# Optimization experiments

Measured on AMD Instinct MI355X. Metric: run time of the kernel, lower is better.

## Reference

```python
import jax, jax.numpy as jnp
import numpy as np

B, N, D, F = 4, 50000, 8, 128

def setup_inputs() -> dict:
    key = jax.random.key(0)
    ks = jax.random.split(key, 6)
    x = jax.random.normal(ks[0], (B, N, F), dtype=jnp.float32)
    adj = jax.random.randint(ks[1], (N, D), 0, N, dtype=jnp.int32)
    # torch.nn.Linear weights: [out_features, in_features], in = 2*F
    W1 = jax.random.normal(ks[2], (F, 2 * F), dtype=jnp.float32) * 0.05
    b1 = jax.random.normal(ks[3], (F,), dtype=jnp.float32) * 0.05
    W2 = jax.random.normal(ks[4], (F, 2 * F), dtype=jnp.float32) * 0.05
    b2 = jax.random.normal(ks[5], (F,), dtype=jnp.float32) * 0.05
    return {"x": x, "adj": adj, "W1": W1, "b1": b1, "W2": W2, "b2": b2}

def _gnn_layer(x, adj, W, b):
    # x: [B, N, F]; adj: [N, D]
    nb = x[:, adj, :]                 # [B, N, D, F] irregular gather
    agg = jnp.max(nb, axis=2)         # max-aggregate over neighbors -> [B, N, F]
    cc = jnp.concatenate([agg, x], axis=-1)  # [B, N, 2F]
    return jax.nn.relu(jnp.einsum('bnf,of->bno', cc, W) + b)

def reference(x, adj, W1, b1, W2, b2):
    x = _gnn_layer(x, adj, W1, b1)
    x = _gnn_layer(x, adj, W2, b2)
    return x
```

## Files before the change

### kernel.cpp

```cpp
#include <hip/hip_runtime.h>


#define N_NODES 50000
#define N_BATCH 4
#define DEG 8
#define FDIM 128
#define K2 256
#define TILE_M 64

typedef _Float16 f16x8 __attribute__((ext_vector_type(8)));
typedef _Float16 f16x4 __attribute__((ext_vector_type(4)));
typedef float f32x4 __attribute__((ext_vector_type(4)));

__global__ void split_w_kernel(const float* __restrict__ W1, const float* __restrict__ W2,
                               _Float16* __restrict__ w1h, _Float16* __restrict__ w1l,
                               _Float16* __restrict__ w2h, _Float16* __restrict__ w2l) {
  const int i = blockIdx.x * 256 + threadIdx.x;
  {
    const float a = W1[i];
    const _Float16 h = (_Float16)a;
    w1h[i] = h;
    w1l[i] = (_Float16)(a - (float)h);
  }
  {
    const float a = W2[i];
    const _Float16 h = (_Float16)a;
    w2h[i] = h;
    w2l[i] = (_Float16)(a - (float)h);
  }
}

__global__ void cvt_x_kernel(const float* __restrict__ x, _Float16* __restrict__ x16) {
  const size_t i = ((size_t)blockIdx.x * 256 + threadIdx.x) * 4;
  const f32x4 v = *(const f32x4*)(x + i);
  f16x4 h;
  #pragma unroll
  for (int j = 0; j < 4; ++j) h[j] = (_Float16)v[j];
  *(f16x4*)(x16 + i) = h;
}

static __device__ inline f16x4 vmax4(f16x4 a, f16x4 b) {
  f16x4 r;
  #pragma unroll
  for (int j = 0; j < 4; ++j) r[j] = a[j] > b[j] ? a[j] : b[j];
  return r;
}

template <bool OUT_F32>
__global__ __launch_bounds__(256, 4)
void gnn_layer_kernel(const _Float16* __restrict__ xin, const int* __restrict__ adj,
                      const _Float16* __restrict__ Wh, const _Float16* __restrict__ Wl,
                      const float* __restrict__ bias, void* __restrict__ out_) {
  __shared__ unsigned char lds[32768];

  const int tid = (int)threadIdx.x;
  const int b   = (int)blockIdx.y;
  const int n0  = (int)blockIdx.x * TILE_M;

  const int l   = tid & 63;
  const int wv  = tid >> 6;
  const int col = l & 15;
  const int kg  = l >> 4;
  const int o0  = wv * 32;

  const int lane32 = tid & 31;
  const int nh     = tid >> 5;
  const _Float16* xb = xin + (size_t)b * N_NODES * FDIM;

  for (int it = 0; it < 8; ++it) {
    const int nl = it * 8 + nh;
    const int ng = n0 + nl;
    f16x4 agg = (f16x4){0, 0, 0, 0};
    f16x4 xv  = (f16x4){0, 0, 0, 0};
    if (ng < N_NODES) {
      const _Float16 ninf = (_Float16)(-65504.0f);
      agg = (f16x4){ninf, ninf, ninf, ninf};
      const int* arow = adj + ng * DEG;
      #pragma unroll
      for (int d = 0; d < DEG; ++d) {
        const int nbr = arow[d];
        const f16x4 v = *(const f16x4*)(xb + (size_t)nbr * FDIM + lane32 * 4);
        agg = vmax4(agg, v);
      }
      xv = *(const f16x4*)(xb + (size_t)ng * FDIM + lane32 * 4);
    }
    const int swz = (nl & 7) << 4;
    *(f16x4*)(lds + nl * 512 + ((lane32 * 8) ^ swz))       = agg;
    *(f16x4*)(lds + nl * 512 + ((256 + lane32 * 8) ^ swz)) = xv;
  }

  __syncthreads();

  f32x4 acc[4][2] = {};
  #pragma unroll
  for (int h2 = 0; h2 < 2; ++h2) {
    #pragma unroll
    for (int kt = 0; kt < 4; ++kt) {
      const int k = h2 * 128 + kt * 32 + kg * 8;
      const f16x8 Bh0 = *(const f16x8*)(Wh + (o0 + col) * K2 + k);
      const f16x8 Bh1 = *(const f16x8*)(Wh + (o0 + 16 + col) * K2 + k);
      const f16x8 Bl0 = *(const f16x8*)(Wl + (o0 + col) * K2 + k);
      const f16x8 Bl1 = *(const f16x8*)(Wl + (o0 + 16 + col) * K2 + k);
      f16x8 Ah[4];
      #pragma unroll
      for (int mf = 0; mf < 4; ++mf) {
        const int row = mf * 16 + col;
        Ah[mf] = *(const f16x8*)(lds + row * 512 + ((k * 2) ^ ((row & 7) << 4)));
      }
      #pragma unroll
      for (int mf = 0; mf < 4; ++mf) {
        acc[mf][0] = __builtin_amdgcn_mfma_f32_16x16x32_f16(Ah[mf], Bh0, acc[mf][0], 0, 0, 0);
        acc[mf][0] = __builtin_amdgcn_mfma_f32_16x16x32_f16(Ah[mf], Bl0, acc[mf][0], 0, 0, 0);
        acc[mf][1] = __builtin_amdgcn_mfma_f32_16x16x32_f16(Ah[mf], Bh1, acc[mf][1], 0, 0, 0);
        acc[mf][1] = __builtin_amdgcn_mfma_f32_16x16x32_f16(Ah[mf], Bl1, acc[mf][1], 0, 0, 0);
      }
    }
  }

  const float bv0 = bias[o0 + col];
  const float bv1 = bias[o0 + 16 + col];
  #pragma unroll
  for (int mf = 0; mf < 4; ++mf) {
    #pragma unroll
    for (int j = 0; j < 4; ++j) {
      const int nl = mf * 16 + kg * 4 + j;
      const int ng = n0 + nl;
      if (ng < N_NODES) {
        const float r0 = fmaxf(acc[mf][0][j] + bv0, 0.f);
        const float r1 = fmaxf(acc[mf][1][j] + bv1, 0.f);
        if (OUT_F32) {
          float* orow = (float*)out_ + ((size_t)b * N_NODES + ng) * FDIM;
          orow[o0 + col]      = r0;
          orow[o0 + 16 + col] = r1;
        } else {
          _Float16* orow = (_Float16*)out_ + ((size_t)b * N_NODES + ng) * FDIM;
          orow[o0 + col]      = (_Float16)r0;
          orow[o0 + 16 + col] = (_Float16)r1;
        }
      }
    }
  }
}

extern "C" void kernel_launch(void* const* d_in, const int* in_sizes, int n_in,
                              void* d_out, int out_size, void* d_ws, size_t ws_size,
                              hipStream_t stream) {
  const float* x  = (const float*)d_in[0];
  const int* adj  = (const int*)d_in[1];
  const float* W1 = (const float*)d_in[2];
  const float* b1 = (const float*)d_in[3];
  const float* W2 = (const float*)d_in[4];
  const float* b2 = (const float*)d_in[5];
  float* out      = (float*)d_out;

  char* ws = (char*)d_ws;
  const size_t nElem = (size_t)N_BATCH * N_NODES * FDIM;
  _Float16* x16   = (_Float16*)ws;
  _Float16* inter = x16 + nElem;
  _Float16* w1h   = inter + nElem;
  _Float16* w1l   = w1h + 32768;
  _Float16* w2h   = w1l + 32768;
  _Float16* w2l   = w2h + 32768;

  split_w_kernel<<<128, 256, 0, stream>>>(W1, W2, w1h, w1l, w2h, w2l);
  cvt_x_kernel<<<25000, 256, 0, stream>>>(x, x16);

  dim3 grid((N_NODES + TILE_M - 1) / TILE_M, N_BATCH);
  gnn_layer_kernel<false><<<grid, 256, 0, stream>>>(x16, adj, w1h, w1l, b1, inter);
  gnn_layer_kernel<true><<<grid, 256, 0, stream>>>(inter, adj, w2h, w2l, b2, out);
}
```

Measured before the change: 414.5 us.

## Interleave batch into node-major fp16 layout so gathers fetch all batches at once

Converts x into an [N, B, F] fp16 layout so each neighbor gather reads a contiguous 1 KB row covering all four batches, and the intermediate is stored in the same layout. Each block now handles 16 nodes across all batches, with 16-byte loads and all eight neighbor loads issued before a tree max, which cuts repeated adjacency reads and raises memory-level parallelism. Final fp32 output uses nontemporal stores, and launch bounds move to 5 waves per SIMD. Bounds checks are removed because N is divisible by 16.

```diff
diff --git a/kernel.cpp b/kernel.cpp
--- a/kernel.cpp
+++ b/kernel.cpp
@@ -6,7 +6,7 @@
 #define DEG 8
 #define FDIM 128
 #define K2 256
-#define TILE_M 64
+#define TILE_N 16
 
 typedef _Float16 f16x8 __attribute__((ext_vector_type(8)));
 typedef _Float16 f16x4 __attribute__((ext_vector_type(4)));
@@ -30,32 +30,38 @@
   }
 }
 
-__global__ void cvt_x_kernel(const float* __restrict__ x, _Float16* __restrict__ x16) {
-  const size_t i = ((size_t)blockIdx.x * 256 + threadIdx.x) * 4;
-  const f32x4 v = *(const f32x4*)(x + i);
-  f16x4 h;
+__global__ void transpose_x_kernel(const float* __restrict__ x, _Float16* __restrict__ xT) {
+  const int wv = threadIdx.x >> 6, l = threadIdx.x & 63;
+  const int n = blockIdx.x * 4 + wv;
+  const int b = l >> 4;
+  const int c8 = (l & 15) * 8;
+  const float* src = x + ((size_t)b * N_NODES + n) * FDIM + c8;
+  const f32x4 v0 = *(const f32x4*)src;
+  const f32x4 v1 = *(const f32x4*)(src + 4);
+  f16x8 h;
   #pragma unroll
-  for (int j = 0; j < 4; ++j) h[j] = (_Float16)v[j];
-  *(f16x4*)(x16 + i) = h;
+  for (int j = 0; j < 4; ++j) h[j] = (_Float16)v0[j];
+  #pragma unroll
+  for (int j = 0; j < 4; ++j) h[4 + j] = (_Float16)v1[j];
+  *(f16x8*)(xT + ((size_t)n * N_BATCH + b) * FDIM + c8) = h;
 }
 
-static __device__ inline f16x4 vmax4(f16x4 a, f16x4 b) {
-  f16x4 r;
+static __device__ inline f16x8 vmax8(f16x8 a, f16x8 b) {
+  f16x8 r;
   #pragma unroll
-  for (int j = 0; j < 4; ++j) r[j] = a[j] > b[j] ? a[j] : b[j];
+  for (int j = 0; j < 8; ++j) r[j] = a[j] > b[j] ? a[j] : b[j];
   return r;
 }
 
 template <bool OUT_F32>
-__global__ __launch_bounds__(256, 4)
-void gnn_layer_kernel(const _Float16* __restrict__ xin, const int* __restrict__ adj,
+__global__ __launch_bounds__(256, 5)
+void gnn_layer_kernel(const _Float16* __restrict__ xT, const int* __restrict__ adj,
                       const _Float16* __restrict__ Wh, const _Float16* __restrict__ Wl,
                       const float* __restrict__ bias, void* __restrict__ out_) {
   __shared__ unsigned char lds[32768];
 
   const int tid = (int)threadIdx.x;
-  const int b   = (int)blockIdx.y;
-  const int n0  = (int)blockIdx.x * TILE_M;
+  const int n0  = (int)blockIdx.x * TILE_N;
 
   const int l   = tid & 63;
   const int wv  = tid >> 6;
@@ -63,30 +69,25 @@
   const int kg  = l >> 4;
   const int o0  = wv * 32;
 
-  const int lane32 = tid & 31;
-  const int nh     = tid >> 5;
-  const _Float16* xb = xin + (size_t)b * N_NODES * FDIM;
-
-  for (int it = 0; it < 8; ++it) {
-    const int nl = it * 8 + nh;
+  const int bb = l >> 4;
+  const int c8 = (l & 15) * 8;
+  #pragma unroll 2
+  for (int i = 0; i < 4; ++i) {
+    const int nl = wv * 4 + i;
     const int ng = n0 + nl;
-    f16x4 agg = (f16x4){0, 0, 0, 0};
-    f16x4 xv  = (f16x4){0, 0, 0, 0};
-    if (ng < N_NODES) {
-      const _Float16 ninf = (_Float16)(-65504.0f);
-      agg = (f16x4){ninf, ninf, ninf, ninf};
-      const int* arow = adj + ng * DEG;
-      #pragma unroll
-      for (int d = 0; d < DEG; ++d) {
-        const int nbr = arow[d];
-        const f16x4 v = *(const f16x4*)(xb + (size_t)nbr * FDIM + lane32 * 4);
-        agg = vmax4(agg, v);
-      }
-      xv = *(const f16x4*)(xb + (size_t)ng * FDIM + lane32 * 4);
-    }
-    const int swz = (nl & 7) << 4;
-    *(f16x4*)(lds + nl * 512 + ((lane32 * 8) ^ swz))       = agg;
-    *(f16x4*)(lds + nl * 512 + ((256 + lane32 * 8) ^ swz)) = xv;
+    const int* arow = adj + ng * DEG;
+    const size_t laneoff = (size_t)bb * FDIM + c8;
+    f16x8 v[DEG];
+    #pragma unroll
+    for (int d = 0; d < DEG; ++d)
+      v[d] = *(const f16x8*)(xT + (size_t)arow[d] * (N_BATCH * FDIM) + laneoff);
+    const f16x8 xv = *(const f16x8*)(xT + (size_t)ng * (N_BATCH * FDIM) + laneoff);
+    const f16x8 agg = vmax8(vmax8(vmax8(v[0], v[1]), vmax8(v[2], v[3])),
+                            vmax8(vmax8(v[4], v[5]), vmax8(v[6], v[7])));
+    const int r   = nl * N_BATCH + bb;
+    const int swz = (r & 7) << 4;
+    *(f16x8*)(lds + r * 512 + ((c8 * 2) ^ swz))       = agg;
+    *(f16x8*)(lds + r * 512 + (256 + ((c8 * 2) ^ swz))) = xv;
   }
 
   __syncthreads();
@@ -105,7 +106,9 @@
       #pragma unroll
       for (int mf = 0; mf < 4; ++mf) {
         const int row = mf * 16 + col;
-        Ah[mf] = *(const f16x8*)(lds + row * 512 + ((k * 2) ^ ((row & 7) << 4)));
+        const int kb  = k * 2;
+        Ah[mf] = *(const f16x8*)(lds + row * 512 +
+                                 ((kb & 256) | ((kb & 255) ^ ((row & 7) << 4))));
       }
       #pragma unroll
       for (int mf = 0; mf < 4; ++mf) {
@@ -123,20 +126,18 @@
   for (int mf = 0; mf < 4; ++mf) {
     #pragma unroll
     for (int j = 0; j < 4; ++j) {
-      const int nl = mf * 16 + kg * 4 + j;
-      const int ng = n0 + nl;
-      if (ng < N_NODES) {
-        const float r0 = fmaxf(acc[mf][0][j] + bv0, 0.f);
-        const float r1 = fmaxf(acc[mf][1][j] + bv1, 0.f);
-        if (OUT_F32) {
-          float* orow = (float*)out_ + ((size_t)b * N_NODES + ng) * FDIM;
-          orow[o0 + col]      = r0;
-          orow[o0 + 16 + col] = r1;
-        } else {
-          _Float16* orow = (_Float16*)out_ + ((size_t)b * N_NODES + ng) * FDIM;
-          orow[o0 + col]      = (_Float16)r0;
-          orow[o0 + 16 + col] = (_Float16)r1;
-        }
+      const int r = mf * 16 + kg * 4 + j;
+      const float r0 = fmaxf(acc[mf][0][j] + bv0, 0.f);
+      const float r1 = fmaxf(acc[mf][1][j] + bv1, 0.f);
+      if (OUT_F32) {
+        const int b = r & 3, n = n0 + (r >> 2);
+        float* orow = (float*)out_ + ((size_t)b * N_NODES + n) * FDIM;
+        __builtin_nontemporal_store(r0, &orow[o0 + col]);
+        __builtin_nontemporal_store(r1, &orow[o0 + 16 + col]);
+      } else {
+        _Float16* orow = (_Float16*)out_ + ((size_t)n0 * N_BATCH + r) * FDIM;
+        orow[o0 + col]      = (_Float16)r0;
+        orow[o0 + 16 + col] = (_Float16)r1;
       }
     }
   }
@@ -155,17 +156,17 @@
 
   char* ws = (char*)d_ws;
   const size_t nElem = (size_t)N_BATCH * N_NODES * FDIM;
-  _Float16* x16   = (_Float16*)ws;
-  _Float16* inter = x16 + nElem;
+  _Float16* xT    = (_Float16*)ws;
+  _Float16* inter = xT + nElem;
   _Float16* w1h   = inter + nElem;
   _Float16* w1l   = w1h + 32768;
   _Float16* w2h   = w1l + 32768;
   _Float16* w2l   = w2h + 32768;
 
   split_w_kernel<<<128, 256, 0, stream>>>(W1, W2, w1h, w1l, w2h, w2l);
-  cvt_x_kernel<<<25000, 256, 0, stream>>>(x, x16);
+  transpose_x_kernel<<<12500, 256, 0, stream>>>(x, xT);
 
-  dim3 grid((N_NODES + TILE_M - 1) / TILE_M, N_BATCH);
-  gnn_layer_kernel<false><<<grid, 256, 0, stream>>>(x16, adj, w1h, w1l, b1, inter);
+  const int grid = N_NODES / TILE_N;
+  gnn_layer_kernel<false><<<grid, 256, 0, stream>>>(xT, adj, w1h, w1l, b1, inter);
   gnn_layer_kernel<true><<<grid, 256, 0, stream>>>(inter, adj, w2h, w2l, b2, out);
 }
```

Result: faster. 363.1 us (-12.4%).
